# Performance work log

Hardware: AMD Instinct MI355X
Metric: run time of the kernel (lower is better)

## Reference

```python
import jax, jax.numpy as jnp
import numpy as np

N, E, G = 50000, 500000, 1024
ND, ED, H, L, OUT = 32, 16, 128, 4, 1
BN_EPS = 1e-5


def setup_inputs() -> dict:
    key = jax.random.key(0)
    ks = jax.random.split(key, 32)

    def w(k, shape, fan):
        return jax.random.normal(k, shape, jnp.float32) / np.float32(np.sqrt(fan))

    inp = {
        "x": jax.random.normal(ks[0], (N, ND), jnp.float32),
        "edge_index": jax.random.randint(ks[1], (2, E), 0, N, jnp.int64),
        "edge_attr": jax.random.normal(ks[2], (E, ED), jnp.float32),
        "batch": jax.random.randint(ks[3], (N,), 0, G, jnp.int64),
        # embeddings
        "ne_w": w(ks[4], (ND, H), ND), "ne_b": jnp.zeros((H,), jnp.float32),
        "ee_w": w(ks[5], (ED, H), ED), "ee_b": jnp.zeros((H,), jnp.float32),
        # per-layer node_mlp: Linear(2H,H) ReLU Linear(H,H) BN(H)
        "nm_w1": w(ks[6], (L, 2 * H, H), 2 * H), "nm_b1": jnp.zeros((L, H), jnp.float32),
        "nm_w2": w(ks[7], (L, H, H), H), "nm_b2": jnp.zeros((L, H), jnp.float32),
        "bn_g": jnp.ones((L, H), jnp.float32), "bn_b": jnp.zeros((L, H), jnp.float32),
        # per-layer edge_mlp: Linear(H,H) ReLU Linear(H,H)  (edge_dim==hidden_dim inside MPNN)
        "em_w1": w(ks[8], (L, H, H), H), "em_b1": jnp.zeros((L, H), jnp.float32),
        "em_w2": w(ks[9], (L, H, H), H), "em_b2": jnp.zeros((L, H), jnp.float32),
        # readout: Linear(H,H) ReLU Dropout(eval=identity) Linear(H,OUT)
        "ro_w1": w(ks[10], (H, H), H), "ro_b1": jnp.zeros((H,), jnp.float32),
        "ro_w2": w(ks[11], (H, OUT), H), "ro_b2": jnp.zeros((OUT,), jnp.float32),
    }
    return inp


def reference(x, edge_index, edge_attr, batch,
              ne_w, ne_b, ee_w, ee_b,
              nm_w1, nm_b1, nm_w2, nm_b2, bn_g, bn_b,
              em_w1, em_b1, em_w2, em_b2,
              ro_w1, ro_b1, ro_w2, ro_b2):
    src, dst = edge_index[0], edge_index[1]  # PyG default: x_j from source, aggregate at target
    h = x @ ne_w + ne_b                      # [N, H]
    e = edge_attr @ ee_w + ee_b              # [E, H]
    inv_std = np.float32(1.0 / np.sqrt(1.0 + BN_EPS))  # eval BN, running_mean=0, running_var=1
    for l in range(nm_w1.shape[0]):
        # edge_mlp
        e = jax.nn.relu(e @ em_w1[l] + em_b1[l]) @ em_w2[l] + em_b2[l]
        # message: concat(x_j, edge_attr) -> node_mlp
        msg = jnp.concatenate([h[src], e], axis=1)              # [E, 2H]
        msg = jax.nn.relu(msg @ nm_w1[l] + nm_b1[l]) @ nm_w2[l] + nm_b2[l]
        msg = msg * (inv_std * bn_g[l]) + bn_b[l]               # BatchNorm1d (eval)
        # scatter-add aggregation + residual update
        agg = jax.ops.segment_sum(msg, dst, num_segments=h.shape[0])
        h = agg + h
    pooled = jax.ops.segment_sum(h, batch, num_segments=G)      # global_add_pool -> [G, H]
    return jax.nn.relu(pooled @ ro_w1 + ro_b1) @ ro_w2 + ro_b2  # [G, OUT]
```

## Files before the change

kernel.cpp:

```cpp
#include <hip/hip_runtime.h>
#include <hip/hip_bf16.h>
#include <math.h>

#define NN 50000
#define EE 500000
#define GG 1024
#define NDIM 32
#define EDIM 16
#define HH 128
#define LL 4
#define NT2 ((EE + 127) / 128)
#define NB2 ((NN + 127) / 128)
#define SCAN_NB ((NN + 255) / 256)

typedef unsigned short ushortT;
typedef __attribute__((ext_vector_type(8))) short bf16x8;
typedef __attribute__((ext_vector_type(4))) float f32x4;

#define MFMA16(a, b, c) __builtin_amdgcn_mfma_f32_16x16x32_bf16(a, b, c, 0, 0, 0)

__device__ inline float bf2f(ushortT u) {
    union { unsigned int i; float f; } v; v.i = ((unsigned int)u) << 16; return v.f;
}
__device__ inline ushortT f2bf(float f) {
    union { float f; unsigned int i; } v; v.f = f;
    unsigned int r = v.i + 0x7FFFu + ((v.i >> 16) & 1u);
    return (ushortT)(r >> 16);
}
__device__ inline short f2bfs(float f) { return (short)f2bf(f); }

__device__ inline bf16x8 lds_a(const char* base, int strideB, int row, int colByte,
                               int mask) {
    int b = row * strideB + colByte;
    b ^= ((row & mask) << 4);
    return *reinterpret_cast<const bf16x8*>(base + b);
}

__global__ __launch_bounds__(256) void hist_kernel(
        const int* __restrict__ dst, int* __restrict__ counts) {
    int i = blockIdx.x * 256 + threadIdx.x;
    if (i < EE) atomicAdd(&counts[dst[i]], 1);
}

__global__ __launch_bounds__(256) void scan_part1(
        const int* __restrict__ counts, int* __restrict__ bsum) {
    __shared__ int buf[256];
    int t = threadIdx.x;
    int i = blockIdx.x * 256 + t;
    buf[t] = (i < NN) ? counts[i] : 0;
    __syncthreads();
    for (int s = 128; s > 0; s >>= 1) {
        if (t < s) buf[t] += buf[t + s];
        __syncthreads();
    }
    if (t == 0) bsum[blockIdx.x] = buf[0];
}

__global__ __launch_bounds__(256) void scan_part2(
        const int* __restrict__ bsum, int* __restrict__ bbase) {
    __shared__ int buf[256];
    int t = threadIdx.x;
    int v = (t < SCAN_NB) ? bsum[t] : 0;
    buf[t] = v;
    __syncthreads();
    for (int off = 1; off < 256; off <<= 1) {
        int s = (t >= off) ? buf[t - off] : 0;
        __syncthreads();
        buf[t] += s;
        __syncthreads();
    }
    if (t < SCAN_NB) bbase[t] = buf[t] - v;
}

__global__ __launch_bounds__(256) void scan_part3(
        const int* __restrict__ counts, const int* __restrict__ bbase,
        int* __restrict__ base) {
    __shared__ int buf[256];
    int t = threadIdx.x;
    int i = blockIdx.x * 256 + t;
    int v = (i < NN) ? counts[i] : 0;
    buf[t] = v;
    __syncthreads();
    for (int off = 1; off < 256; off <<= 1) {
        int s = (t >= off) ? buf[t - off] : 0;
        __syncthreads();
        buf[t] += s;
        __syncthreads();
    }
    if (i < NN) base[i] = bbase[blockIdx.x] + buf[t] - v;
}

__global__ __launch_bounds__(256) void build_perm_kernel(
        const int* __restrict__ src, const int* __restrict__ dst,
        const int* __restrict__ base, int* __restrict__ cnt,
        int* __restrict__ perm, int* __restrict__ srcS, int* __restrict__ dstS) {
    int i = blockIdx.x * 256 + threadIdx.x;
    if (i >= EE) return;
    int d = dst[i];
    int pos = base[d] + atomicAdd(&cnt[d], 1);
    perm[pos] = i;
    srcS[pos] = src[i];
    dstS[pos] = d;
}

__global__ __launch_bounds__(256) void transpose_kernel(
        const float* __restrict__ in, ushortT* __restrict__ out, int K, int N) {
    int per = K * N;
    int total = LL * per;
    int idx = blockIdx.x * 256 + threadIdx.x;
    if (idx >= total) return;
    int l = idx / per, rem = idx - l * per;
    int n = rem / K, k = rem - n * K;
    out[idx] = f2bf(in[(size_t)l * per + (size_t)k * N + n]);
}

__global__ __launch_bounds__(256) void transpose_ee_kernel(
        const float* __restrict__ in, ushortT* __restrict__ out) {
    int idx = blockIdx.x * 256 + threadIdx.x;
    if (idx >= HH * 32) return;
    int n = idx >> 5, k = idx & 31;
    out[idx] = (k < EDIM) ? f2bf(in[k * HH + n]) : (ushortT)0;
}

__global__ __launch_bounds__(256) void bnfold_kernel(
        const float* __restrict__ w2, const float* __restrict__ b2,
        const float* __restrict__ bng, const float* __restrict__ bnb,
        ushortT* __restrict__ w2g, float* __restrict__ nb2g, float inv_std) {
    int idx = blockIdx.x * 256 + threadIdx.x;
    if (idx < LL * HH * HH) {
        int l = idx / (HH * HH), rem = idx - l * (HH * HH);
        int n = rem / HH, k = rem - n * HH;
        w2g[idx] = f2bf(w2[(size_t)l * HH * HH + (size_t)k * HH + n] *
                        bng[l * HH + n] * inv_std);
    }
    if (idx < LL * HH) {
        nb2g[idx] = b2[idx] * bng[idx] * inv_std + bnb[idx];
    }
}

__global__ __launch_bounds__(128) void node_embed_kernel(
        const float* __restrict__ x, const float* __restrict__ w,
        const float* __restrict__ b, float* __restrict__ h) {
    __shared__ float xs[NDIM];
    int i = blockIdx.x, j = threadIdx.x;
    if (j < NDIM) xs[j] = x[(size_t)i * NDIM + j];
    __syncthreads();
    float acc = b[j];
#pragma unroll
    for (int k = 0; k < NDIM; ++k) acc += xs[k] * w[k * HH + j];
    h[(size_t)i * HH + j] = acc;
}

template<int K, int KS, bool HASB>
__device__ inline void gemm_b(const char* aBase, int aStrideB, int aMask,
        const ushortT* __restrict__ wT, const float* __restrict__ bias,
        int wr, int wc, int l15, int lg, f32x4 acc[2][4]) {
#pragma unroll
    for (int ntl = 0; ntl < 4; ++ntl) {
        float bb = HASB ? bias[wc * 64 + ntl * 16 + l15] : 0.f;
        f32x4 iv = {bb, bb, bb, bb};
        acc[0][ntl] = iv;
        acc[1][ntl] = iv;
    }
#pragma unroll
    for (int ks = 0; ks < K / 32; ++ks) {
        int kk = ks * 32 + lg * 8;
        bf16x8 a0 = lds_a(aBase, aStrideB, wr * 32 + l15,      kk * 2, aMask);
        bf16x8 a1 = lds_a(aBase, aStrideB, wr * 32 + 16 + l15, kk * 2, aMask);
#pragma unroll
        for (int ntl = 0; ntl < 4; ++ntl) {
            int n = wc * 64 + ntl * 16 + l15;
            bf16x8 b = *reinterpret_cast<const bf16x8*>(wT + (size_t)n * KS + kk);
            acc[0][ntl] = MFMA16(a0, b, acc[0][ntl]);
            acc[1][ntl] = MFMA16(a1, b, acc[1][ntl]);
        }
    }
}

__device__ inline void gemm_uinit3(const char* aBase, const char* uBase,
        const ushortT* __restrict__ wT,
        int wr, int wc, int l15, int lg, f32x4 acc[2][4]) {
#pragma unroll
    for (int mt = 0; mt < 2; ++mt)
#pragma unroll
        for (int ntl = 0; ntl < 4; ++ntl) {
            int col = wc * 64 + ntl * 16 + l15;
#pragma unroll
            for (int r = 0; r < 4; ++r) {
                int row = wr * 32 + mt * 16 + lg * 4 + r;
                int b = row * 256 + col * 2; b ^= ((row & 7) << 4);
                acc[mt][ntl][r] = bf2f(*reinterpret_cast<const ushortT*>(uBase + b));
            }
        }
#pragma unroll
    for (int ks = 0; ks < 4; ++ks) {
        int kk = ks * 32 + lg * 8;
        bf16x8 a0 = lds_a(aBase, 256, wr * 32 + l15,      kk * 2, 7);
        bf16x8 a1 = lds_a(aBase, 256, wr * 32 + 16 + l15, kk * 2, 7);
#pragma unroll
        for (int ntl = 0; ntl < 4; ++ntl) {
            int n = wc * 64 + ntl * 16 + l15;
            bf16x8 b = *reinterpret_cast<const bf16x8*>(wT + (size_t)n * 256 + kk);
            acc[0][ntl] = MFMA16(a0, b, acc[0][ntl]);
            acc[1][ntl] = MFMA16(a1, b, acc[1][ntl]);
        }
    }
}

__device__ inline void wfrag(char* base, int wr, int wc, int l15, int lg,
                             f32x4 acc[2][4], bool relu) {
#pragma unroll
    for (int mt = 0; mt < 2; ++mt)
#pragma unroll
        for (int ntl = 0; ntl < 4; ++ntl) {
            int col = wc * 64 + ntl * 16 + l15;
#pragma unroll
            for (int r = 0; r < 4; ++r) {
                int row = wr * 32 + mt * 16 + lg * 4 + r;
                int b = row * 256 + col * 2;
                b ^= ((row & 7) << 4);
                float v = acc[mt][ntl][r];
                if (relu) v = fmaxf(v, 0.f);
                *reinterpret_cast<ushortT*>(base + b) = f2bf(v);
            }
        }
}

template<int EMBED, int LASTL>
__global__ __launch_bounds__(512) void edgeA_kernel(
        const ushortT* __restrict__ u, ushortT* __restrict__ e,
        const int* __restrict__ srcS, const int* __restrict__ dstS,
        const int* __restrict__ basep, const int* __restrict__ perm,
        const float* __restrict__ ea,
        const ushortT* __restrict__ eewT, const float* __restrict__ eeb,
        const ushortT* __restrict__ ew1t, const float* __restrict__ eb1,
        const ushortT* __restrict__ ew2t, const float* __restrict__ eb2,
        const ushortT* __restrict__ nw1bt,
        ushortT* __restrict__ partials) {
    __shared__ __align__(16) char eT[128 * 256];
    __shared__ __align__(16) char uT[128 * 256];
    __shared__ int dstx[128], bstartL[128], sidx[128], pidx[128];

    const int e0 = blockIdx.x * 128;
    int V = EE - e0; if (V > 128) V = 128;
    const int tid = threadIdx.x;
    const bf16x8 z8 = {0, 0, 0, 0, 0, 0, 0, 0};

    if (tid < 128) {
        int ii = e0 + tid;
        int d = (ii < EE) ? dstS[ii] : -1;
        dstx[tid] = d;
        bstartL[tid] = (d >= 0) ? basep[d] : 0;
        sidx[tid] = (ii < EE) ? srcS[ii] : 0;
        if (EMBED) pidx[tid] = (ii < EE) ? perm[ii] : 0;
    }
    __syncthreads();

#pragma unroll
    for (int s = 0; s < 4; ++s) {
        int idx = tid + s * 512;
        int row = idx >> 4, c8 = (idx & 15) * 8;
        bf16x8 v = *reinterpret_cast<const bf16x8*>(u + (size_t)sidx[row] * HH + c8);
        int b = row * 256 + c8 * 2; b ^= ((row & 7) << 4);
        *reinterpret_cast<bf16x8*>(uT + b) = v;
    }
    if (EMBED) {
        {
            int row = tid >> 2, q4 = (tid & 3) * 4;
            float4 v = *reinterpret_cast<const float4*>(
                ea + (size_t)pidx[row] * EDIM + q4);
            unsigned long long pack =
                (unsigned long long)f2bf(v.x) |
                ((unsigned long long)f2bf(v.y) << 16) |
                ((unsigned long long)f2bf(v.z) << 32) |
                ((unsigned long long)f2bf(v.w) << 48);
            int b = row * 64 + q4 * 2; b ^= ((row & 3) << 4);
            *reinterpret_cast<unsigned long long*>(eT + b) = pack;
        }
        if (tid < 256) {
            int row = tid >> 1;
            int b = row * 64 + 32 + (tid & 1) * 16; b ^= ((row & 3) << 4);
            *reinterpret_cast<bf16x8*>(eT + b) = z8;
        }
    } else {
#pragma unroll
        for (int s = 0; s < 4; ++s) {
            int idx = tid + s * 512;
            int row = idx >> 4, c8 = (idx & 15) * 8;
            bf16x8 v = *reinterpret_cast<const bf16x8*>(
                e + (size_t)(e0 + row) * HH + c8);
            int b = row * 256 + c8 * 2; b ^= ((row & 7) << 4);
            *reinterpret_cast<bf16x8*>(eT + b) = v;
        }
    }
    __syncthreads();

    const int wid = tid >> 6, lane = tid & 63;
    const int wr = wid >> 1, wc = wid & 1, l15 = lane & 15, lg = lane >> 4;
    f32x4 acc[2][4];

    if (EMBED) {
        gemm_b<32, 32, true>(eT, 64, 3, eewT, eeb, wr, wc, l15, lg, acc);
        __syncthreads();
        wfrag(eT, wr, wc, l15, lg, acc, false);
        __syncthreads();
    }
    gemm_b<HH, HH, true>(eT, 256, 7, ew1t, eb1, wr, wc, l15, lg, acc);
    __syncthreads();
    wfrag(eT, wr, wc, l15, lg, acc, true);
    __syncthreads();
    gemm_b<HH, HH, true>(eT, 256, 7, ew2t, eb2, wr, wc, l15, lg, acc);
    __syncthreads();
    wfrag(eT, wr, wc, l15, lg, acc, false);
    __syncthreads();
    if (!LASTL) {
#pragma unroll
        for (int s = 0; s < 4; ++s) {
            int idx = tid + s * 512;
            int row = idx >> 4, c8 = (idx & 15) * 8;
            if (row < V) {
                int b = row * 256 + c8 * 2; b ^= ((row & 7) << 4);
                *reinterpret_cast<bf16x8*>(e + (size_t)(e0 + row) * HH + c8) =
                    *reinterpret_cast<const bf16x8*>(eT + b);
            }
        }
    }
    gemm_uinit3(eT, uT, nw1bt, wr, wc, l15, lg, acc);
    __syncthreads();
    wfrag(eT, wr, wc, l15, lg, acc, true);
    __syncthreads();

    {
        int col = tid & 127, seg = tid >> 7;
        int r = seg * 32, rend = r + 32;
        float sum = 0.f;
        int dprev = -1, runStart = r;
        for (; r < rend; ++r) {
            int d = dstx[r];
            if (d != dprev) {
                if (dprev >= 0) {
                    int slot = ((e0 + runStart) >> 5) - (bstartL[runStart] >> 5);
                    if (slot < 3)
                        partials[((size_t)slot * NN + dprev) * HH + col] = f2bf(sum);
                }
                sum = 0.f; dprev = d; runStart = r;
            }
            if (d >= 0) {
                int b = r * 256 + col * 2; b ^= ((r & 7) << 4);
                sum += bf2f(*reinterpret_cast<const ushortT*>(eT + b));
            }
        }
        if (dprev >= 0) {
            int slot = ((e0 + runStart) >> 5) - (bstartL[runStart] >> 5);
            if (slot < 3)
                partials[((size_t)slot * NN + dprev) * HH + col] = f2bf(sum);
        }
    }
}

template<int HASU>
__global__ __launch_bounds__(512) void nodeB_kernel(
        const ushortT* __restrict__ partials, const int* __restrict__ basep,
        const ushortT* __restrict__ w2g, const float* __restrict__ nb2g,
        float* __restrict__ h,
        const ushortT* __restrict__ w1tn, const float* __restrict__ b1n,
        ushortT* __restrict__ uOut) {
    __shared__ __align__(16) char sT[128 * 256];
    __shared__ int degx[128];
    const int n0 = blockIdx.x * 128;
    int V = NN - n0; if (V > 128) V = 128;
    const int tid = threadIdx.x;

    __shared__ int basex[128];
    if (tid < 128) {
        int bs = 0, de = 0;
        if (tid < V) {
            int n = n0 + tid;
            bs = basep[n];
            int be = (n + 1 < NN) ? basep[n + 1] : EE;
            de = be - bs;
        }
        basex[tid] = bs;
        degx[tid] = de;
    }
    __syncthreads();

#pragma unroll
    for (int g = 0; g < 4; ++g) {
        int node = g * 32 + (tid >> 4);
        int c8 = (tid & 15) * 8;
        float s[8] = {0.f, 0.f, 0.f, 0.f, 0.f, 0.f, 0.f, 0.f};
        if (node < V) {
            int bs = basex[node], de = degx[node];
            if (de > 0) {
                int ns = ((bs + de - 1) >> 5) - (bs >> 5) + 1;
                if (ns > 3) ns = 3;
                for (int sl = 0; sl < ns; ++sl) {
                    bf16x8 pv = *reinterpret_cast<const bf16x8*>(
                        partials + ((size_t)sl * NN + n0 + node) * HH + c8);
#pragma unroll
                    for (int j = 0; j < 8; ++j) s[j] += bf2f((ushortT)pv[j]);
                }
            }
        }
        bf16x8 o;
#pragma unroll
        for (int j = 0; j < 8; ++j) o[j] = f2bfs(s[j]);
        int b = node * 256 + c8 * 2; b ^= ((node & 7) << 4);
        *reinterpret_cast<bf16x8*>(sT + b) = o;
    }
    __syncthreads();

    const int wid = tid >> 6, lane = tid & 63;
    const int wr = wid >> 1, wc = wid & 1, l15 = lane & 15, lg = lane >> 4;
    f32x4 acc[2][4];

    gemm_b<HH, HH, false>(sT, 256, 7, w2g, nullptr, wr, wc, l15, lg, acc);
#pragma unroll
    for (int ntl = 0; ntl < 4; ++ntl) {
        int col = wc * 64 + ntl * 16 + l15;
        float bg = nb2g[col];
#pragma unroll
        for (int mt = 0; mt < 2; ++mt)
#pragma unroll
            for (int r = 0; r < 4; ++r) {
                int row = wr * 32 + mt * 16 + lg * 4 + r;
                if (row < V) {
                    size_t off = (size_t)(n0 + row) * HH + col;
                    float hn = h[off] + acc[mt][ntl][r] + (float)degx[row] * bg;
                    h[off] = hn;
                    acc[mt][ntl][r] = hn;
                } else {
                    acc[mt][ntl][r] = 0.f;
                }
            }
    }
    if (HASU) {
        __syncthreads();
        wfrag(sT, wr, wc, l15, lg, acc, false);
        __syncthreads();
        gemm_b<HH, 2 * HH, true>(sT, 256, 7, w1tn, b1n, wr, wc, l15, lg, acc);
        __syncthreads();
        wfrag(sT, wr, wc, l15, lg, acc, false);
        __syncthreads();
#pragma unroll
        for (int s = 0; s < 4; ++s) {
            int idx = tid + s * 512;
            int row = idx >> 4, c8 = (idx & 15) * 8;
            if (row < V) {
                int b = row * 256 + c8 * 2; b ^= ((row & 7) << 4);
                *reinterpret_cast<bf16x8*>(uOut + (size_t)(n0 + row) * HH + c8) =
                    *reinterpret_cast<const bf16x8*>(sT + b);
            }
        }
    }
}

__global__ __launch_bounds__(512) void node_pre_kernel(
        const float* __restrict__ h, const ushortT* __restrict__ w1t,
        const float* __restrict__ b1, ushortT* __restrict__ uo) {
    __shared__ __align__(16) char sT[128 * 256];
    const int n0 = blockIdx.x * 128;
    int V = NN - n0; if (V > 128) V = 128;
    const int tid = threadIdx.x;
#pragma unroll
    for (int s = 0; s < 4; ++s) {
        int idx = tid + s * 512;
        int row = idx >> 4, c8 = (idx & 15) * 8;
        bf16x8 o = {0, 0, 0, 0, 0, 0, 0, 0};
        if (row < V) {
            const float* hp = h + (size_t)(n0 + row) * HH + c8;
            float4 va = *reinterpret_cast<const float4*>(hp);
            float4 vb = *reinterpret_cast<const float4*>(hp + 4);
            o[0] = f2bfs(va.x); o[1] = f2bfs(va.y); o[2] = f2bfs(va.z); o[3] = f2bfs(va.w);
            o[4] = f2bfs(vb.x); o[5] = f2bfs(vb.y); o[6] = f2bfs(vb.z); o[7] = f2bfs(vb.w);
        }
        int b = row * 256 + c8 * 2; b ^= ((row & 7) << 4);
        *reinterpret_cast<bf16x8*>(sT + b) = o;
    }
    __syncthreads();
    const int wid = tid >> 6, lane = tid & 63;
    const int wr = wid >> 1, wc = wid & 1, l15 = lane & 15, lg = lane >> 4;
    f32x4 acc[2][4];
    gemm_b<HH, 2 * HH, true>(sT, 256, 7, w1t, b1, wr, wc, l15, lg, acc);
    __syncthreads();
    wfrag(sT, wr, wc, l15, lg, acc, false);
    __syncthreads();
#pragma unroll
    for (int s = 0; s < 4; ++s) {
        int idx = tid + s * 512;
        int row = idx >> 4, c8 = (idx & 15) * 8;
        if (row < V) {
            int b = row * 256 + c8 * 2; b ^= ((row & 7) << 4);
            *reinterpret_cast<bf16x8*>(uo + (size_t)(n0 + row) * HH + c8) =
                *reinterpret_cast<const bf16x8*>(sT + b);
        }
    }
}

__global__ __launch_bounds__(256) void pool_kernel(
        const float* __restrict__ h, const int* __restrict__ batch,
        float* __restrict__ pooled) {
    long long idx = (long long)blockIdx.x * 256 + threadIdx.x;
    if (idx >= (long long)NN * HH) return;
    int i = (int)(idx >> 7), c = (int)(idx & 127);
    atomicAdd(&pooled[(size_t)batch[i] * HH + c], h[idx]);
}

__global__ __launch_bounds__(128) void readout_kernel(
        const float* __restrict__ pooled,
        const float* __restrict__ w1, const float* __restrict__ b1,
        const float* __restrict__ w2, const float* __restrict__ b2,
        float* __restrict__ out) {
    __shared__ float row[HH];
    __shared__ float red[HH];
    int g = blockIdx.x, j = threadIdx.x;
    row[j] = pooled[(size_t)g * HH + j];
    __syncthreads();
    float acc = b1[j];
    for (int k = 0; k < HH; ++k) acc += row[k] * w1[k * HH + j];
    red[j] = fmaxf(acc, 0.f) * w2[j];
    __syncthreads();
    for (int s = 64; s > 0; s >>= 1) {
        if (j < s) red[j] += red[j + s];
        __syncthreads();
    }
    if (j == 0) out[g] = red[0] + b2[0];
}

extern "C" void kernel_launch(void* const* d_in, const int* in_sizes, int n_in,
                              void* d_out, int out_size, void* d_ws, size_t ws_size,
                              hipStream_t stream) {
    const float* x     = (const float*)d_in[0];
    const int*   ei    = (const int*)d_in[1];
    const float* ea    = (const float*)d_in[2];
    const int*   batch = (const int*)d_in[3];
    const float* ne_w  = (const float*)d_in[4];
    const float* ne_b  = (const float*)d_in[5];
    const float* ee_w  = (const float*)d_in[6];
    const float* ee_b  = (const float*)d_in[7];
    const float* nm_w1 = (const float*)d_in[8];
    const float* nm_b1 = (const float*)d_in[9];
    const float* nm_w2 = (const float*)d_in[10];
    const float* nm_b2 = (const float*)d_in[11];
    const float* bn_g  = (const float*)d_in[12];
    const float* bn_b  = (const float*)d_in[13];
    const float* em_w1 = (const float*)d_in[14];
    const float* em_b1 = (const float*)d_in[15];
    const float* em_w2 = (const float*)d_in[16];
    const float* em_b2 = (const float*)d_in[17];
    const float* ro_w1 = (const float*)d_in[18];
    const float* ro_b1 = (const float*)d_in[19];
    const float* ro_w2 = (const float*)d_in[20];
    const float* ro_b2 = (const float*)d_in[21];

    const int* srcp = ei;
    const int* dstp = ei + EE;

    char* p = (char*)d_ws;
    float* h = (float*)p;            p += (size_t)NN * HH * 4;
    float* pooled = (float*)p;       p += (size_t)GG * HH * 4;
    ushortT* ebuf = (ushortT*)p;     p += (size_t)EE * HH * 2;
    ushortT* ubuf = (ushortT*)p;     p += (size_t)NN * HH * 2;
    ushortT* partials = (ushortT*)p; p += (size_t)3 * NN * HH * 2;
    ushortT* ew1t = (ushortT*)p;     p += (size_t)LL * HH * HH * 2;
    ushortT* ew2t = (ushortT*)p;     p += (size_t)LL * HH * HH * 2;
    ushortT* nw1t = (ushortT*)p;     p += (size_t)LL * 2 * HH * HH * 2;
    ushortT* w2g  = (ushortT*)p;     p += (size_t)LL * HH * HH * 2;
    float* nb2g   = (float*)p;       p += (size_t)LL * HH * 4;
    ushortT* eewT = (ushortT*)p;     p += (size_t)HH * 32 * 2;
    int* perm   = (int*)p;           p += (size_t)EE * 4;
    int* srcS   = (int*)p;           p += (size_t)EE * 4;
    int* dstS   = (int*)p;           p += (size_t)EE * 4;
    int* counts = (int*)p;           p += (size_t)NN * 4;
    int* basep  = (int*)p;           p += (size_t)NN * 4;
    int* cnt    = (int*)p;           p += (size_t)NN * 4;
    int* bsum   = (int*)p;           p += (size_t)SCAN_NB * 4;
    int* bbase  = (int*)p;           p += (size_t)SCAN_NB * 4;

    hipMemsetAsync(counts, 0, (size_t)NN * 4, stream);
    hipMemsetAsync(cnt, 0, (size_t)NN * 4, stream);
    hist_kernel<<<(EE + 255) / 256, 256, 0, stream>>>(dstp, counts);
    scan_part1<<<SCAN_NB, 256, 0, stream>>>(counts, bsum);
    scan_part2<<<1, 256, 0, stream>>>(bsum, bbase);
    scan_part3<<<SCAN_NB, 256, 0, stream>>>(counts, bbase, basep);
    build_perm_kernel<<<(EE + 255) / 256, 256, 0, stream>>>(
        srcp, dstp, basep, cnt, perm, srcS, dstS);

    const float inv_std = 1.0f / sqrtf(1.0f + 1e-5f);
    transpose_kernel<<<(LL * HH * HH + 255) / 256, 256, 0, stream>>>(em_w1, ew1t, HH, HH);
    transpose_kernel<<<(LL * HH * HH + 255) / 256, 256, 0, stream>>>(em_w2, ew2t, HH, HH);
    transpose_kernel<<<(LL * 2 * HH * HH + 255) / 256, 256, 0, stream>>>(nm_w1, nw1t, 2 * HH, HH);
    bnfold_kernel<<<(LL * HH * HH + 255) / 256, 256, 0, stream>>>(
        nm_w2, nm_b2, bn_g, bn_b, w2g, nb2g, inv_std);
    transpose_ee_kernel<<<(HH * 32 + 255) / 256, 256, 0, stream>>>(ee_w, eewT);

    node_embed_kernel<<<NN, 128, 0, stream>>>(x, ne_w, ne_b, h);
    node_pre_kernel<<<NB2, 512, 0, stream>>>(h, nw1t, nm_b1, ubuf);

    for (int l = 0; l < LL; ++l) {
        const ushortT* nw1bt = nw1t + (size_t)l * 2 * HH * HH + 128;
        if (l == 0) {
            edgeA_kernel<1, 0><<<NT2, 512, 0, stream>>>(
                ubuf, ebuf, srcS, dstS, basep, perm, ea, eewT, ee_b,
                ew1t + (size_t)l * HH * HH, em_b1 + l * HH,
                ew2t + (size_t)l * HH * HH, em_b2 + l * HH,
                nw1bt, partials);
        } else if (l < LL - 1) {
            edgeA_kernel<0, 0><<<NT2, 512, 0, stream>>>(
                ubuf, ebuf, srcS, dstS, basep, perm, ea, eewT, ee_b,
                ew1t + (size_t)l * HH * HH, em_b1 + l * HH,
                ew2t + (size_t)l * HH * HH, em_b2 + l * HH,
                nw1bt, partials);
        } else {
            edgeA_kernel<0, 1><<<NT2, 512, 0, stream>>>(
                ubuf, ebuf, srcS, dstS, basep, perm, ea, eewT, ee_b,
                ew1t + (size_t)l * HH * HH, em_b1 + l * HH,
                ew2t + (size_t)l * HH * HH, em_b2 + l * HH,
                nw1bt, partials);
        }
        if (l < LL - 1) {
            nodeB_kernel<1><<<NB2, 512, 0, stream>>>(
                partials, basep, w2g + (size_t)l * HH * HH, nb2g + l * HH, h,
                nw1t + (size_t)(l + 1) * 2 * HH * HH, nm_b1 + (l + 1) * HH, ubuf);
        } else {
            nodeB_kernel<0><<<NB2, 512, 0, stream>>>(
                partials, basep, w2g + (size_t)l * HH * HH, nb2g + l * HH, h,
                nw1t, nm_b1, ubuf);
        }
    }

    hipMemsetAsync(pooled, 0, sizeof(float) * (size_t)GG * HH, stream);
    {
        long long total = (long long)NN * HH;
        pool_kernel<<<(int)((total + 255) / 256), 256, 0, stream>>>(h, batch, pooled);
    }
    readout_kernel<<<GG, 128, 0, stream>>>(pooled, ro_w1, ro_b1, ro_w2, ro_b2,
                                           (float*)d_out);
}
```

Measured before the change: 1.196 ms.

## Shrink edge tile to 64 rows, gather source rows into registers, ping-pong LDS

The edge kernel now handles 64 edges per block with 256 threads instead of 128 edges with 512 threads. The gathered source-node features go straight into per-lane registers in MFMA accumulator layout instead of a second LDS tile. Two LDS buffers alternate between GEMM stages, which drops several barriers. This cuts LDS per block to allow more resident blocks and overlaps the gather with setup, at the cost of more registers per thread and more blocks, each with a shorter per-destination partial-sum run.

```diff
diff --git a/kernel.cpp b/kernel.cpp
--- a/kernel.cpp
+++ b/kernel.cpp
@@ -9,7 +9,7 @@
 #define EDIM 16
 #define HH 128
 #define LL 4
-#define NT2 ((EE + 127) / 128)
+#define NT64 ((EE + 63) / 64)
 #define NB2 ((NN + 127) / 128)
 #define SCAN_NB ((NN + 255) / 256)
 
@@ -177,36 +177,6 @@
     }
 }
 
-__device__ inline void gemm_uinit3(const char* aBase, const char* uBase,
-        const ushortT* __restrict__ wT,
-        int wr, int wc, int l15, int lg, f32x4 acc[2][4]) {
-#pragma unroll
-    for (int mt = 0; mt < 2; ++mt)
-#pragma unroll
-        for (int ntl = 0; ntl < 4; ++ntl) {
-            int col = wc * 64 + ntl * 16 + l15;
-#pragma unroll
-            for (int r = 0; r < 4; ++r) {
-                int row = wr * 32 + mt * 16 + lg * 4 + r;
-                int b = row * 256 + col * 2; b ^= ((row & 7) << 4);
-                acc[mt][ntl][r] = bf2f(*reinterpret_cast<const ushortT*>(uBase + b));
-            }
-        }
-#pragma unroll
-    for (int ks = 0; ks < 4; ++ks) {
-        int kk = ks * 32 + lg * 8;
-        bf16x8 a0 = lds_a(aBase, 256, wr * 32 + l15,      kk * 2, 7);
-        bf16x8 a1 = lds_a(aBase, 256, wr * 32 + 16 + l15, kk * 2, 7);
-#pragma unroll
-        for (int ntl = 0; ntl < 4; ++ntl) {
-            int n = wc * 64 + ntl * 16 + l15;
-            bf16x8 b = *reinterpret_cast<const bf16x8*>(wT + (size_t)n * 256 + kk);
-            acc[0][ntl] = MFMA16(a0, b, acc[0][ntl]);
-            acc[1][ntl] = MFMA16(a1, b, acc[1][ntl]);
-        }
-    }
-}
-
 __device__ inline void wfrag(char* base, int wr, int wc, int l15, int lg,
                              f32x4 acc[2][4], bool relu) {
 #pragma unroll
@@ -227,7 +197,7 @@
 }
 
 template<int EMBED, int LASTL>
-__global__ __launch_bounds__(512) void edgeA_kernel(
+__global__ __launch_bounds__(256) void edgeA_kernel(
         const ushortT* __restrict__ u, ushortT* __restrict__ e,
         const int* __restrict__ srcS, const int* __restrict__ dstS,
         const int* __restrict__ basep, const int* __restrict__ perm,
@@ -237,33 +207,39 @@
         const ushortT* __restrict__ ew2t, const float* __restrict__ eb2,
         const ushortT* __restrict__ nw1bt,
         ushortT* __restrict__ partials) {
-    __shared__ __align__(16) char eT[128 * 256];
-    __shared__ __align__(16) char uT[128 * 256];
-    __shared__ int dstx[128], bstartL[128], sidx[128], pidx[128];
-
-    const int e0 = blockIdx.x * 128;
-    int V = EE - e0; if (V > 128) V = 128;
+    __shared__ __align__(16) char eT[64 * 256];
+    __shared__ __align__(16) char hidM[64 * 256];
+    __shared__ int dstx[64], bstartL[64], pidx[EMBED ? 64 : 1];
+
+    const int e0 = blockIdx.x * 64;
+    int V = EE - e0; if (V > 64) V = 64;
     const int tid = threadIdx.x;
+    const int wid = tid >> 6, lane = tid & 63;
+    const int wr = wid >> 1, wc = wid & 1, l15 = lane & 15, lg = lane >> 4;
     const bf16x8 z8 = {0, 0, 0, 0, 0, 0, 0, 0};
 
-    if (tid < 128) {
+    unsigned short ureg[2][4][4];
+#pragma unroll
+    for (int mt = 0; mt < 2; ++mt)
+#pragma unroll
+        for (int r = 0; r < 4; ++r) {
+            int grow = e0 + wr * 32 + mt * 16 + lg * 4 + r;
+            int s = (grow < EE) ? srcS[grow] : 0;
+            const ushortT* up = u + (size_t)s * HH + wc * 64 + l15;
+#pragma unroll
+            for (int ntl = 0; ntl < 4; ++ntl)
+                ureg[mt][ntl][r] = up[ntl * 16];
+        }
+
+    if (tid < 64) {
         int ii = e0 + tid;
         int d = (ii < EE) ? dstS[ii] : -1;
         dstx[tid] = d;
         bstartL[tid] = (d >= 0) ? basep[d] : 0;
-        sidx[tid] = (ii < EE) ? srcS[ii] : 0;
         if (EMBED) pidx[tid] = (ii < EE) ? perm[ii] : 0;
     }
     __syncthreads();
 
-#pragma unroll
-    for (int s = 0; s < 4; ++s) {
-        int idx = tid + s * 512;
-        int row = idx >> 4, c8 = (idx & 15) * 8;
-        bf16x8 v = *reinterpret_cast<const bf16x8*>(u + (size_t)sidx[row] * HH + c8);
-        int b = row * 256 + c8 * 2; b ^= ((row & 7) << 4);
-        *reinterpret_cast<bf16x8*>(uT + b) = v;
-    }
     if (EMBED) {
         {
             int row = tid >> 2, q4 = (tid & 3) * 4;
@@ -275,17 +251,17 @@
                 ((unsigned long long)f2bf(v.z) << 32) |
                 ((unsigned long long)f2bf(v.w) << 48);
             int b = row * 64 + q4 * 2; b ^= ((row & 3) << 4);
-            *reinterpret_cast<unsigned long long*>(eT + b) = pack;
-        }
-        if (tid < 256) {
+            *reinterpret_cast<unsigned long long*>(hidM + b) = pack;
+        }
+        if (tid < 128) {
             int row = tid >> 1;
             int b = row * 64 + 32 + (tid & 1) * 16; b ^= ((row & 3) << 4);
-            *reinterpret_cast<bf16x8*>(eT + b) = z8;
+            *reinterpret_cast<bf16x8*>(hidM + b) = z8;
         }
     } else {
 #pragma unroll
         for (int s = 0; s < 4; ++s) {
-            int idx = tid + s * 512;
+            int idx = tid + s * 256;
             int row = idx >> 4, c8 = (idx & 15) * 8;
             bf16x8 v = *reinterpret_cast<const bf16x8*>(
                 e + (size_t)(e0 + row) * HH + c8);
@@ -295,28 +271,22 @@
     }
     __syncthreads();
 
-    const int wid = tid >> 6, lane = tid & 63;
-    const int wr = wid >> 1, wc = wid & 1, l15 = lane & 15, lg = lane >> 4;
     f32x4 acc[2][4];
-
     if (EMBED) {
-        gemm_b<32, 32, true>(eT, 64, 3, eewT, eeb, wr, wc, l15, lg, acc);
-        __syncthreads();
+        gemm_b<32, 32, true>(hidM, 64, 3, eewT, eeb, wr, wc, l15, lg, acc);
         wfrag(eT, wr, wc, l15, lg, acc, false);
         __syncthreads();
     }
     gemm_b<HH, HH, true>(eT, 256, 7, ew1t, eb1, wr, wc, l15, lg, acc);
-    __syncthreads();
-    wfrag(eT, wr, wc, l15, lg, acc, true);
-    __syncthreads();
-    gemm_b<HH, HH, true>(eT, 256, 7, ew2t, eb2, wr, wc, l15, lg, acc);
-    __syncthreads();
+    wfrag(hidM, wr, wc, l15, lg, acc, true);
+    __syncthreads();
+    gemm_b<HH, HH, true>(hidM, 256, 7, ew2t, eb2, wr, wc, l15, lg, acc);
     wfrag(eT, wr, wc, l15, lg, acc, false);
     __syncthreads();
     if (!LASTL) {
 #pragma unroll
         for (int s = 0; s < 4; ++s) {
-            int idx = tid + s * 512;
+            int idx = tid + s * 256;
             int row = idx >> 4, c8 = (idx & 15) * 8;
             if (row < V) {
                 int b = row * 256 + c8 * 2; b ^= ((row & 7) << 4);
@@ -325,9 +295,27 @@
             }
         }
     }
-    gemm_uinit3(eT, uT, nw1bt, wr, wc, l15, lg, acc);
-    __syncthreads();
-    wfrag(eT, wr, wc, l15, lg, acc, true);
+#pragma unroll
+    for (int mt = 0; mt < 2; ++mt)
+#pragma unroll
+        for (int ntl = 0; ntl < 4; ++ntl)
+#pragma unroll
+            for (int r = 0; r < 4; ++r)
+                acc[mt][ntl][r] = bf2f(ureg[mt][ntl][r]);
+#pragma unroll
+    for (int ks = 0; ks < 4; ++ks) {
+        int kk = ks * 32 + lg * 8;
+        bf16x8 a0 = lds_a(eT, 256, wr * 32 + l15,      kk * 2, 7);
+        bf16x8 a1 = lds_a(eT, 256, wr * 32 + 16 + l15, kk * 2, 7);
+#pragma unroll
+        for (int ntl = 0; ntl < 4; ++ntl) {
+            int n = wc * 64 + ntl * 16 + l15;
+            bf16x8 b = *reinterpret_cast<const bf16x8*>(nw1bt + (size_t)n * 256 + kk);
+            acc[0][ntl] = MFMA16(a0, b, acc[0][ntl]);
+            acc[1][ntl] = MFMA16(a1, b, acc[1][ntl]);
+        }
+    }
+    wfrag(hidM, wr, wc, l15, lg, acc, true);
     __syncthreads();
 
     {
@@ -347,7 +335,7 @@
             }
             if (d >= 0) {
                 int b = r * 256 + col * 2; b ^= ((r & 7) << 4);
-                sum += bf2f(*reinterpret_cast<const ushortT*>(eT + b));
+                sum += bf2f(*reinterpret_cast<const ushortT*>(hidM + b));
             }
         }
         if (dprev >= 0) {
@@ -367,11 +355,11 @@
         ushortT* __restrict__ uOut) {
     __shared__ __align__(16) char sT[128 * 256];
     __shared__ int degx[128];
+    __shared__ int basex[128];
     const int n0 = blockIdx.x * 128;
     int V = NN - n0; if (V > 128) V = 128;
     const int tid = threadIdx.x;
 
-    __shared__ int basex[128];
     if (tid < 128) {
         int bs = 0, de = 0;
         if (tid < V) {
@@ -601,19 +589,19 @@
     for (int l = 0; l < LL; ++l) {
         const ushortT* nw1bt = nw1t + (size_t)l * 2 * HH * HH + 128;
         if (l == 0) {
-            edgeA_kernel<1, 0><<<NT2, 512, 0, stream>>>(
+            edgeA_kernel<1, 0><<<NT64, 256, 0, stream>>>(
                 ubuf, ebuf, srcS, dstS, basep, perm, ea, eewT, ee_b,
                 ew1t + (size_t)l * HH * HH, em_b1 + l * HH,
                 ew2t + (size_t)l * HH * HH, em_b2 + l * HH,
                 nw1bt, partials);
         } else if (l < LL - 1) {
-            edgeA_kernel<0, 0><<<NT2, 512, 0, stream>>>(
+            edgeA_kernel<0, 0><<<NT64, 256, 0, stream>>>(
                 ubuf, ebuf, srcS, dstS, basep, perm, ea, eewT, ee_b,
                 ew1t + (size_t)l * HH * HH, em_b1 + l * HH,
                 ew2t + (size_t)l * HH * HH, em_b2 + l * HH,
                 nw1bt, partials);
         } else {
-            edgeA_kernel<0, 1><<<NT2, 512, 0, stream>>>(
+            edgeA_kernel<0, 1><<<NT64, 256, 0, stream>>>(
                 ubuf, ebuf, srcS, dstS, basep, perm, ea, eewT, ee_b,
                 ew1t + (size_t)l * HH * HH, em_b1 + l * HH,
                 ew2t + (size_t)l * HH * HH, em_b2 + l * HH,
```

Result: slower. 1.315 ms (+9.9%).
